# Optimization experiments

Hardware: AMD Instinct MI355X
Metric: run time of the kernel (lower is better)

Reference implementation:

```python
import jax, jax.numpy as jnp
import numpy as np

H = 16        # hidden_dim
L = 2         # n_layers
B = 1048576   # batch


def _mlp(x, W1, b1, W2, b2):
    # Linear -> ReLU -> Linear
    return jnp.maximum(x @ W1 + b1, 0.0) @ W2 + b2


def setup_inputs() -> dict:
    key = jax.random.key(0)
    ks = iter(jax.random.split(key, 40))

    def p(shape, scale=0.25):
        return (jax.random.normal(next(ks), shape, dtype=jnp.float32) * scale)

    inp = {
        "node_features": jax.random.normal(next(ks), (B, 2, 2), dtype=jnp.float32),
        "edge_distance_3d": jax.random.uniform(next(ks), (B,), dtype=jnp.float32),
        "edge_delta_z": jax.random.normal(next(ks), (B,), dtype=jnp.float32),
        "edge_sin_2delta_phi": jax.random.normal(next(ks), (B,), dtype=jnp.float32),
        # node embed MLP: 2 -> H -> H
        "ne_W1": p((2, H)), "ne_b1": p((H,)), "ne_W2": p((H, H)), "ne_b2": p((H,)),
        # edge embed MLP: 3 -> H -> H
        "ee_W1": p((3, H)), "ee_b1": p((H,)), "ee_W2": p((H, H)), "ee_b2": p((H,)),
        # per-layer message MLP: (2H+H)=48 -> H -> H, stacked over L layers
        "msg_W1": p((L, 3 * H, H)), "msg_b1": p((L, H)),
        "msg_W2": p((L, H, H)), "msg_b2": p((L, H)),
        # per-layer update MLP: 2H -> H -> H
        "upd_W1": p((L, 2 * H, H)), "upd_b1": p((L, H)),
        "upd_W2": p((L, H, H)), "upd_b2": p((L, H)),
        # classifier: H -> H -> 1
        "cls_W1": p((H, H)), "cls_b1": p((H,)),
        "cls_W2": p((H, 1)), "cls_b2": p((1,)),
    }
    return inp


def reference(node_features, edge_distance_3d, edge_delta_z, edge_sin_2delta_phi,
              ne_W1, ne_b1, ne_W2, ne_b2,
              ee_W1, ee_b1, ee_W2, ee_b2,
              msg_W1, msg_b1, msg_W2, msg_b2,
              upd_W1, upd_b1, upd_W2, upd_b2,
              cls_W1, cls_b1, cls_W2, cls_b2):
    batch = node_features.shape[0]
    # node embedding: flatten (B,2,2) -> (2B,2), embed, back to (B,2,H)
    node_embed = _mlp(node_features.reshape(-1, node_features.shape[-1]),
                      ne_W1, ne_b1, ne_W2, ne_b2).reshape(batch, 2, H)
    edge_input = jnp.stack([edge_distance_3d, edge_delta_z, edge_sin_2delta_phi], axis=-1)  # (B,3)
    edge_embed = _mlp(edge_input, ee_W1, ee_b1, ee_W2, ee_b2)  # (B,H)

    h = node_embed
    n_layers = msg_W1.shape[0]
    for l in range(n_layers):
        n0, n1 = h[:, 0, :], h[:, 1, :]
        msg_01 = _mlp(jnp.concatenate([n0, n1, edge_embed], axis=-1),
                      msg_W1[l], msg_b1[l], msg_W2[l], msg_b2[l])
        msg_10 = _mlp(jnp.concatenate([n1, n0, edge_embed], axis=-1),
                      msg_W1[l], msg_b1[l], msg_W2[l], msg_b2[l])
        upd_0 = _mlp(jnp.concatenate([n0, msg_01], axis=-1),
                     upd_W1[l], upd_b1[l], upd_W2[l], upd_b2[l])
        upd_1 = _mlp(jnp.concatenate([n1, msg_10], axis=-1),
                     upd_W1[l], upd_b1[l], upd_W2[l], upd_b2[l])
        h = h + jnp.stack([upd_0, upd_1], axis=1)

    graph_embed = h.mean(axis=1)  # (B,H)
    logits = _mlp(graph_embed, cls_W1, cls_b1, cls_W2, cls_b2).squeeze(-1)  # (B,)
    return logits
```

## Files before the change

kernel.cpp:

```cpp
#include <hip/hip_runtime.h>
#include <hip/hip_bf16.h>

typedef __attribute__((ext_vector_type(8))) short    s8v;
typedef __attribute__((ext_vector_type(4))) float    f4v;
typedef __attribute__((ext_vector_type(4))) unsigned u4v;

__device__ __forceinline__ unsigned short bfu(float x){
  union { __hip_bfloat16 h; unsigned short u; } cv;
  cv.h = __float2bfloat16(x);
  return cv.u;
}
__device__ __forceinline__ unsigned pkbf(float lo, float hi){
  return (unsigned)bfu(lo) | ((unsigned)bfu(hi) << 16);
}
__device__ __forceinline__ s8v mkfrag(unsigned a, unsigned b, unsigned c_, unsigned d){
  u4v u = {a, b, c_, d};
  return __builtin_bit_cast(s8v, u);
}
__device__ __forceinline__ f4v MM(s8v a, s8v b, f4v acc){
  return __builtin_amdgcn_mfma_f32_16x16x32_bf16(a, b, acc, 0, 0, 0);
}

struct Pk { unsigned p0, p1; };
template<bool RELU>
__device__ __forceinline__ Pk mkpk(f4v d){
  float a = d[0], b = d[1], c_ = d[2], e = d[3];
  if (RELU){ a = fmaxf(a,0.f); b = fmaxf(b,0.f); c_ = fmaxf(c_,0.f); e = fmaxf(e,0.f); }
  Pk r; r.p0 = pkbf(a, b); r.p1 = pkbf(c_, e); return r;
}

__device__ __forceinline__ s8v bfragK16(Pk x){ return mkfrag(x.p0, x.p1, 0u, 0u); }
__device__ __forceinline__ s8v bfragCat(Pk x, Pk y){ return mkfrag(x.p0, x.p1, y.p0, y.p1); }

__device__ __forceinline__ s8v loadA16(const float* __restrict__ W, int K, int c, int g,
                                       float scale = 1.0f){
  int r0 = 4*g;
  unsigned u0 = pkbf(r0+0<K ? W[(r0+0)*16+c]*scale : 0.f, r0+1<K ? W[(r0+1)*16+c]*scale : 0.f);
  unsigned u1 = pkbf(r0+2<K ? W[(r0+2)*16+c]*scale : 0.f, r0+3<K ? W[(r0+3)*16+c]*scale : 0.f);
  return mkfrag(u0, u1, 0u, 0u);
}
__device__ __forceinline__ s8v loadA32(const float* __restrict__ W, int c, int g){
  int r0 = 4*g;
  unsigned u0 = pkbf(W[(r0+0)*16+c],      W[(r0+1)*16+c]);
  unsigned u1 = pkbf(W[(r0+2)*16+c],      W[(r0+3)*16+c]);
  unsigned u2 = pkbf(W[(16+r0+0)*16+c],   W[(16+r0+1)*16+c]);
  unsigned u3 = pkbf(W[(16+r0+2)*16+c],   W[(16+r0+3)*16+c]);
  return mkfrag(u0, u1, u2, u3);
}
__device__ __forceinline__ f4v ldb(const float* __restrict__ b, int g){
  f4v v; v[0] = b[4*g+0]; v[1] = b[4*g+1]; v[2] = b[4*g+2]; v[3] = b[4*g+3];
  return v;
}

__device__ __forceinline__ void pl32(unsigned &a, unsigned &b){
  asm("v_permlane32_swap_b32 %0, %1" : "+v"(a), "+v"(b));
}
__device__ __forceinline__ void pl16(unsigned &a, unsigned &b){
  asm("v_permlane16_swap_b32 %0, %1" : "+v"(a), "+v"(b));
}

__global__ void __launch_bounds__(256) egnn_zs(
    const float* __restrict__ nf,   const float* __restrict__ dist,
    const float* __restrict__ dz,   const float* __restrict__ s2p,
    const float* __restrict__ neW1, const float* __restrict__ neb1,
    const float* __restrict__ neW2, const float* __restrict__ neb2,
    const float* __restrict__ eeW1, const float* __restrict__ eeb1,
    const float* __restrict__ eeW2, const float* __restrict__ eeb2,
    const float* __restrict__ msgW1, const float* __restrict__ msgb1,
    const float* __restrict__ msgW2, const float* __restrict__ msgb2,
    const float* __restrict__ updW1, const float* __restrict__ updb1,
    const float* __restrict__ updW2, const float* __restrict__ updb2,
    const float* __restrict__ clsW1, const float* __restrict__ clsb1,
    const float* __restrict__ clsW2, const float* __restrict__ clsb2,
    float* __restrict__ out, int B, int ngroups, int nwaves)
{
  const int lane = threadIdx.x & 63;
  const int c = lane & 15;
  const int g = lane >> 4;
  const int gwave = blockIdx.x * (blockDim.x >> 6) + (threadIdx.x >> 6);

  s8v aNe1 = loadA16(neW1, 2, c, g);
  s8v aNe2 = loadA16(neW2, 16, c, g);
  s8v aEe1 = loadA16(eeW1, 3, c, g);
  s8v aEe2 = loadA16(eeW2, 16, c, g);
  s8v aCl  = loadA16(clsW1, 16, c, g, 0.5f);
  s8v aM0[2], aM1[2], aM2[2], aU1[2], aU2[2];
  f4v bM1[2], bM2[2], bU1[2], bU2[2];
  #pragma unroll
  for (int l = 0; l < 2; ++l){
    aM0[l] = loadA32(msgW1 + l*768, c, g);
    aM1[l] = loadA16(msgW1 + l*768 + 512, 16, c, g);
    aM2[l] = loadA16(msgW2 + l*256, 16, c, g);
    aU1[l] = loadA32(updW1 + l*512, c, g);
    aU2[l] = loadA16(updW2 + l*256, 16, c, g);
    bM1[l] = ldb(msgb1 + l*16, g);
    bM2[l] = ldb(msgb2 + l*16, g);
    bU1[l] = ldb(updb1 + l*16, g);
    bU2[l] = ldb(updb2 + l*16, g);
  }
  f4v bNe1 = ldb(neb1,g), bNe2 = ldb(neb2,g), bEe1 = ldb(eeb1,g), bEe2 = ldb(eeb2,g), bCl1 = ldb(clsb1,g);
  const float w2a = clsW2[4*g+0], w2b = clsW2[4*g+1], w2c = clsW2[4*g+2], w2d = clsW2[4*g+3];
  const float cb2 = clsb2[0];

  int grp = gwave;
  float4 nfe = {0,0,0,0}; float di = 0, zz = 0, sp = 0;
  if (grp < ngroups){
    int e = min(grp*16 + c, B-1);
    nfe = *reinterpret_cast<const float4*>(nf + (size_t)e * 4);
    di = dist[e]; zz = dz[e]; sp = s2p[e];
  }

  #pragma unroll 1
  for (; grp < ngroups; grp += nwaves){
    const int e0 = grp * 16;
    float4 nfeN = nfe; float diN = di, zzN = zz, spN = sp;
    const int nxt = grp + nwaves;
    if (nxt < ngroups){
      int e = min(nxt*16 + c, B-1);
      nfeN = *reinterpret_cast<const float4*>(nf + (size_t)e * 4);
      diN = dist[e]; zzN = dz[e]; spN = s2p[e];
    }

    s8v b0 = mkfrag(g==0 ? pkbf(nfe.x, nfe.y) : 0u, 0u, 0u, 0u);
    s8v b1 = mkfrag(g==0 ? pkbf(nfe.z, nfe.w) : 0u, 0u, 0u, 0u);
    s8v be = mkfrag(g==0 ? pkbf(di, zz) : 0u, g==0 ? pkbf(sp, 0.f) : 0u, 0u, 0u);
    f4v t0 = MM(aNe1, b0, bNe1);
    f4v t1 = MM(aNe1, b1, bNe1);
    f4v te = MM(aEe1, be, bEe1);
    f4v h0 = MM(aNe2, bfragK16(mkpk<true>(t0)), bNe2);
    f4v h1 = MM(aNe2, bfragK16(mkpk<true>(t1)), bNe2);
    f4v ee = MM(aEe2, bfragK16(mkpk<true>(te)), bEe2);
    const s8v eeB = bfragK16(mkpk<false>(ee));

    #pragma unroll
    for (int l = 0; l < 2; ++l){
      Pk ph0 = mkpk<false>(h0), ph1 = mkpk<false>(h1);
      f4v eC = MM(aM1[l], eeB, bM1[l]);
      f4v m0 = MM(aM0[l], bfragCat(ph0, ph1), eC);
      f4v m1 = MM(aM0[l], bfragCat(ph1, ph0), eC);
      f4v g0 = MM(aM2[l], bfragK16(mkpk<true>(m0)), bM2[l]);
      f4v g1 = MM(aM2[l], bfragK16(mkpk<true>(m1)), bM2[l]);
      f4v u0 = MM(aU1[l], bfragCat(ph0, mkpk<false>(g0)), bU1[l]);
      f4v u1 = MM(aU1[l], bfragCat(ph1, mkpk<false>(g1)), bU1[l]);
      h0 = h0 + MM(aU2[l], bfragK16(mkpk<true>(u0)), bU2[l]);
      h1 = h1 + MM(aU2[l], bfragK16(mkpk<true>(u1)), bU2[l]);
    }

    f4v gb = h0 + h1;
    f4v tc = MM(aCl, bfragK16(mkpk<false>(gb)), bCl1);
    float part = fmaxf(tc[0],0.f)*w2a + fmaxf(tc[1],0.f)*w2b
               + fmaxf(tc[2],0.f)*w2c + fmaxf(tc[3],0.f)*w2d;
    unsigned pu = __builtin_bit_cast(unsigned, part), pv = pu;
    pl16(pu, pv);
    part = __builtin_bit_cast(float, pu) + __builtin_bit_cast(float, pv);
    pu = __builtin_bit_cast(unsigned, part); pv = pu;
    pl32(pu, pv);
    part = __builtin_bit_cast(float, pu) + __builtin_bit_cast(float, pv);
    if (lane < 16 && (e0 + c) < B) out[e0 + c] = part + cb2;

    nfe = nfeN; di = diN; zz = zzN; sp = spN;
  }
}

extern "C" void kernel_launch(void* const* d_in, const int* in_sizes, int n_in,
                              void* d_out, int out_size, void* d_ws, size_t ws_size,
                              hipStream_t stream) {
  const float* nf    = (const float*)d_in[0];
  const float* dist  = (const float*)d_in[1];
  const float* dz    = (const float*)d_in[2];
  const float* s2p   = (const float*)d_in[3];
  const float* neW1  = (const float*)d_in[4];
  const float* neb1  = (const float*)d_in[5];
  const float* neW2  = (const float*)d_in[6];
  const float* neb2  = (const float*)d_in[7];
  const float* eeW1  = (const float*)d_in[8];
  const float* eeb1  = (const float*)d_in[9];
  const float* eeW2  = (const float*)d_in[10];
  const float* eeb2  = (const float*)d_in[11];
  const float* msgW1 = (const float*)d_in[12];
  const float* msgb1 = (const float*)d_in[13];
  const float* msgW2 = (const float*)d_in[14];
  const float* msgb2 = (const float*)d_in[15];
  const float* updW1 = (const float*)d_in[16];
  const float* updb1 = (const float*)d_in[17];
  const float* updW2 = (const float*)d_in[18];
  const float* updb2 = (const float*)d_in[19];
  const float* clsW1 = (const float*)d_in[20];
  const float* clsb1 = (const float*)d_in[21];
  const float* clsW2 = (const float*)d_in[22];
  const float* clsb2 = (const float*)d_in[23];

  const int B = in_sizes[1];
  const int ngroups = (B + 15) / 16;
  int blocks = 1024;
  const int wpb = 256 / 64;
  if (blocks * wpb > ngroups) blocks = (ngroups + wpb - 1) / wpb;
  const int nwaves = blocks * wpb;

  egnn_zs<<<blocks, 256, 0, stream>>>(
      nf, dist, dz, s2p,
      neW1, neb1, neW2, neb2,
      eeW1, eeb1, eeW2, eeb2,
      msgW1, msgb1, msgW2, msgb2,
      updW1, updb1, updW2, updb2,
      clsW1, clsb1, clsW2, clsb2,
      (float*)d_out, B, ngroups, nwaves);
}
```

Baseline: 64.18 us.

## Process two 16-edge groups per wave iteration to interleave independent MFMA chains

Each wave now handles a pair of 16-row groups per loop iteration, interleaving the two independent MFMA dependency chains so matrix-core latency is hidden by instruction-level parallelism. The software prefetch of the next group's inputs is removed, and loads are issued directly at the top of each iteration. The grid doubles to 2048 blocks and launch bounds request 2 blocks per SM. Register pressure roughly doubles for activations, which may reduce occupancy, and exposed load latency returns without the prefetch.

```diff
diff --git a/kernel.cpp b/kernel.cpp
--- a/kernel.cpp
+++ b/kernel.cpp
@@ -58,8 +58,16 @@
 __device__ __forceinline__ void pl16(unsigned &a, unsigned &b){
   asm("v_permlane16_swap_b32 %0, %1" : "+v"(a), "+v"(b));
 }
-
-__global__ void __launch_bounds__(256) egnn_zs(
+__device__ __forceinline__ float qsum(float part){
+  unsigned pu = __builtin_bit_cast(unsigned, part), pv = pu;
+  pl16(pu, pv);
+  part = __builtin_bit_cast(float, pu) + __builtin_bit_cast(float, pv);
+  pu = __builtin_bit_cast(unsigned, part); pv = pu;
+  pl32(pu, pv);
+  return __builtin_bit_cast(float, pu) + __builtin_bit_cast(float, pv);
+}
+
+__global__ void __launch_bounds__(256, 2) egnn_ilp2(
     const float* __restrict__ nf,   const float* __restrict__ dist,
     const float* __restrict__ dz,   const float* __restrict__ s2p,
     const float* __restrict__ neW1, const float* __restrict__ neb1,
@@ -72,7 +80,7 @@
     const float* __restrict__ updW2, const float* __restrict__ updb2,
     const float* __restrict__ clsW1, const float* __restrict__ clsb1,
     const float* __restrict__ clsW2, const float* __restrict__ clsb2,
-    float* __restrict__ out, int B, int ngroups, int nwaves)
+    float* __restrict__ out, int B, int npairs, int nwaves)
 {
   const int lane = threadIdx.x & 63;
   const int c = lane & 15;
@@ -102,63 +110,71 @@
   const float w2a = clsW2[4*g+0], w2b = clsW2[4*g+1], w2c = clsW2[4*g+2], w2d = clsW2[4*g+3];
   const float cb2 = clsb2[0];
 
-  int grp = gwave;
-  float4 nfe = {0,0,0,0}; float di = 0, zz = 0, sp = 0;
-  if (grp < ngroups){
-    int e = min(grp*16 + c, B-1);
-    nfe = *reinterpret_cast<const float4*>(nf + (size_t)e * 4);
-    di = dist[e]; zz = dz[e]; sp = s2p[e];
-  }
-
   #pragma unroll 1
-  for (; grp < ngroups; grp += nwaves){
-    const int e0 = grp * 16;
-    float4 nfeN = nfe; float diN = di, zzN = zz, spN = sp;
-    const int nxt = grp + nwaves;
-    if (nxt < ngroups){
-      int e = min(nxt*16 + c, B-1);
-      nfeN = *reinterpret_cast<const float4*>(nf + (size_t)e * 4);
-      diN = dist[e]; zzN = dz[e]; spN = s2p[e];
-    }
-
-    s8v b0 = mkfrag(g==0 ? pkbf(nfe.x, nfe.y) : 0u, 0u, 0u, 0u);
-    s8v b1 = mkfrag(g==0 ? pkbf(nfe.z, nfe.w) : 0u, 0u, 0u, 0u);
-    s8v be = mkfrag(g==0 ? pkbf(di, zz) : 0u, g==0 ? pkbf(sp, 0.f) : 0u, 0u, 0u);
-    f4v t0 = MM(aNe1, b0, bNe1);
-    f4v t1 = MM(aNe1, b1, bNe1);
-    f4v te = MM(aEe1, be, bEe1);
-    f4v h0 = MM(aNe2, bfragK16(mkpk<true>(t0)), bNe2);
-    f4v h1 = MM(aNe2, bfragK16(mkpk<true>(t1)), bNe2);
-    f4v ee = MM(aEe2, bfragK16(mkpk<true>(te)), bEe2);
-    const s8v eeB = bfragK16(mkpk<false>(ee));
+  for (int p = gwave; p < npairs; p += nwaves){
+    const int e0A = (2*p)     * 16;
+    const int e0B = (2*p + 1) * 16;
+    const int eA = min(e0A + c, B-1);
+    const int eB = min(e0B + c, B-1);
+    const float4 nfA = *reinterpret_cast<const float4*>(nf + (size_t)eA * 4);
+    const float4 nfB = *reinterpret_cast<const float4*>(nf + (size_t)eB * 4);
+    const float diA = dist[eA], zzA = dz[eA], spA = s2p[eA];
+    const float diB = dist[eB], zzB = dz[eB], spB = s2p[eB];
+
+    s8v bA0 = mkfrag(g==0 ? pkbf(nfA.x, nfA.y) : 0u, 0u, 0u, 0u);
+    s8v bB0 = mkfrag(g==0 ? pkbf(nfB.x, nfB.y) : 0u, 0u, 0u, 0u);
+    s8v bA1 = mkfrag(g==0 ? pkbf(nfA.z, nfA.w) : 0u, 0u, 0u, 0u);
+    s8v bB1 = mkfrag(g==0 ? pkbf(nfB.z, nfB.w) : 0u, 0u, 0u, 0u);
+    s8v beA = mkfrag(g==0 ? pkbf(diA, zzA) : 0u, g==0 ? pkbf(spA, 0.f) : 0u, 0u, 0u);
+    s8v beB = mkfrag(g==0 ? pkbf(diB, zzB) : 0u, g==0 ? pkbf(spB, 0.f) : 0u, 0u, 0u);
+    f4v tA0 = MM(aNe1, bA0, bNe1);   f4v tB0 = MM(aNe1, bB0, bNe1);
+    f4v tA1 = MM(aNe1, bA1, bNe1);   f4v tB1 = MM(aNe1, bB1, bNe1);
+    f4v teA = MM(aEe1, beA, bEe1);   f4v teB = MM(aEe1, beB, bEe1);
+    f4v hA0 = MM(aNe2, bfragK16(mkpk<true>(tA0)), bNe2);
+    f4v hB0 = MM(aNe2, bfragK16(mkpk<true>(tB0)), bNe2);
+    f4v hA1 = MM(aNe2, bfragK16(mkpk<true>(tA1)), bNe2);
+    f4v hB1 = MM(aNe2, bfragK16(mkpk<true>(tB1)), bNe2);
+    f4v eeA = MM(aEe2, bfragK16(mkpk<true>(teA)), bEe2);
+    f4v eeB = MM(aEe2, bfragK16(mkpk<true>(teB)), bEe2);
+    const s8v efA = bfragK16(mkpk<false>(eeA));
+    const s8v efB = bfragK16(mkpk<false>(eeB));
 
     #pragma unroll
     for (int l = 0; l < 2; ++l){
-      Pk ph0 = mkpk<false>(h0), ph1 = mkpk<false>(h1);
-      f4v eC = MM(aM1[l], eeB, bM1[l]);
-      f4v m0 = MM(aM0[l], bfragCat(ph0, ph1), eC);
-      f4v m1 = MM(aM0[l], bfragCat(ph1, ph0), eC);
-      f4v g0 = MM(aM2[l], bfragK16(mkpk<true>(m0)), bM2[l]);
-      f4v g1 = MM(aM2[l], bfragK16(mkpk<true>(m1)), bM2[l]);
-      f4v u0 = MM(aU1[l], bfragCat(ph0, mkpk<false>(g0)), bU1[l]);
-      f4v u1 = MM(aU1[l], bfragCat(ph1, mkpk<false>(g1)), bU1[l]);
-      h0 = h0 + MM(aU2[l], bfragK16(mkpk<true>(u0)), bU2[l]);
-      h1 = h1 + MM(aU2[l], bfragK16(mkpk<true>(u1)), bU2[l]);
+      Pk pA0 = mkpk<false>(hA0), pA1 = mkpk<false>(hA1);
+      Pk pB0 = mkpk<false>(hB0), pB1 = mkpk<false>(hB1);
+      f4v eCA = MM(aM1[l], efA, bM1[l]);
+      f4v eCB = MM(aM1[l], efB, bM1[l]);
+      f4v mA0 = MM(aM0[l], bfragCat(pA0, pA1), eCA);
+      f4v mB0 = MM(aM0[l], bfragCat(pB0, pB1), eCB);
+      f4v mA1 = MM(aM0[l], bfragCat(pA1, pA0), eCA);
+      f4v mB1 = MM(aM0[l], bfragCat(pB1, pB0), eCB);
+      f4v gA0 = MM(aM2[l], bfragK16(mkpk<true>(mA0)), bM2[l]);
+      f4v gB0 = MM(aM2[l], bfragK16(mkpk<true>(mB0)), bM2[l]);
+      f4v gA1 = MM(aM2[l], bfragK16(mkpk<true>(mA1)), bM2[l]);
+      f4v gB1 = MM(aM2[l], bfragK16(mkpk<true>(mB1)), bM2[l]);
+      f4v uA0 = MM(aU1[l], bfragCat(pA0, mkpk<false>(gA0)), bU1[l]);
+      f4v uB0 = MM(aU1[l], bfragCat(pB0, mkpk<false>(gB0)), bU1[l]);
+      f4v uA1 = MM(aU1[l], bfragCat(pA1, mkpk<false>(gA1)), bU1[l]);
+      f4v uB1 = MM(aU1[l], bfragCat(pB1, mkpk<false>(gB1)), bU1[l]);
+      hA0 = hA0 + MM(aU2[l], bfragK16(mkpk<true>(uA0)), bU2[l]);
+      hB0 = hB0 + MM(aU2[l], bfragK16(mkpk<true>(uB0)), bU2[l]);
+      hA1 = hA1 + MM(aU2[l], bfragK16(mkpk<true>(uA1)), bU2[l]);
+      hB1 = hB1 + MM(aU2[l], bfragK16(mkpk<true>(uB1)), bU2[l]);
     }
 
-    f4v gb = h0 + h1;
-    f4v tc = MM(aCl, bfragK16(mkpk<false>(gb)), bCl1);
-    float part = fmaxf(tc[0],0.f)*w2a + fmaxf(tc[1],0.f)*w2b
-               + fmaxf(tc[2],0.f)*w2c + fmaxf(tc[3],0.f)*w2d;
-    unsigned pu = __builtin_bit_cast(unsigned, part), pv = pu;
-    pl16(pu, pv);
-    part = __builtin_bit_cast(float, pu) + __builtin_bit_cast(float, pv);
-    pu = __builtin_bit_cast(unsigned, part); pv = pu;
-    pl32(pu, pv);
-    part = __builtin_bit_cast(float, pu) + __builtin_bit_cast(float, pv);
-    if (lane < 16 && (e0 + c) < B) out[e0 + c] = part + cb2;
-
-    nfe = nfeN; di = diN; zz = zzN; sp = spN;
+    f4v tcA = MM(aCl, bfragK16(mkpk<false>(hA0 + hA1)), bCl1);
+    f4v tcB = MM(aCl, bfragK16(mkpk<false>(hB0 + hB1)), bCl1);
+    float prA = fmaxf(tcA[0],0.f)*w2a + fmaxf(tcA[1],0.f)*w2b
+              + fmaxf(tcA[2],0.f)*w2c + fmaxf(tcA[3],0.f)*w2d;
+    float prB = fmaxf(tcB[0],0.f)*w2a + fmaxf(tcB[1],0.f)*w2b
+              + fmaxf(tcB[2],0.f)*w2c + fmaxf(tcB[3],0.f)*w2d;
+    prA = qsum(prA);
+    prB = qsum(prB);
+    if (lane < 16){
+      if (e0A + c < B) out[e0A + c] = prA + cb2;
+      if (e0B + c < B) out[e0B + c] = prB + cb2;
+    }
   }
 }
 
@@ -192,17 +208,18 @@
 
   const int B = in_sizes[1];
   const int ngroups = (B + 15) / 16;
-  int blocks = 1024;
+  const int npairs  = (ngroups + 1) / 2;
+  int blocks = 2048;
   const int wpb = 256 / 64;
-  if (blocks * wpb > ngroups) blocks = (ngroups + wpb - 1) / wpb;
+  if (blocks * wpb > npairs) blocks = (npairs + wpb - 1) / wpb;
   const int nwaves = blocks * wpb;
 
-  egnn_zs<<<blocks, 256, 0, stream>>>(
+  egnn_ilp2<<<blocks, 256, 0, stream>>>(
       nf, dist, dz, s2p,
       neW1, neb1, neW2, neb2,
       eeW1, eeb1, eeW2, eeb2,
       msgW1, msgb1, msgW2, msgb2,
       updW1, updb1, updW2, updb2,
       clsW1, clsb1, clsW2, clsb2,
-      (float*)d_out, B, ngroups, nwaves);
-}
+      (float*)d_out, B, npairs, nwaves);
+}
```

Result: faster. 61.51 us (-4.2%).
